# Performance work log

Measured on AMD Instinct MI355X. Metric: run time of the kernel, lower is better.

Reference implementation:

```python
import jax, jax.numpy as jnp
import numpy as np

NUM_KERNELS = 6
ALPHA = 0.5
DIL = 9
FEAT = 4
DELTA_V = 0.5
DELTA_D = 1.5
EMB_W = 0.25
MAX_LABELS = 16


def setup_inputs() -> dict:
    key = jax.random.key(0)
    k1, k2, k3, k4, k5 = jax.random.split(key, 5)
    B, H, W = 8, 640, 640
    pred = jax.random.normal(k1, (B, NUM_KERNELS + FEAT, H, W), dtype=jnp.float32)
    gt_text = (jax.random.uniform(k2, (B, 1, H, W)) < 0.3).astype(jnp.float32)
    gt_kernels = (jax.random.uniform(k3, (B, NUM_KERNELS - 1, H, W)) < 0.2).astype(jnp.float32)
    training_mask = (jax.random.uniform(k4, (B, 1, H, W)) > 0.05).astype(jnp.float32)
    gt_instance = jax.random.randint(k5, (B, H, W), 0, MAX_LABELS, dtype=jnp.int32)
    return {"pred": pred, "gt_text": gt_text, "gt_kernels": gt_kernels,
            "training_mask": training_mask, "gt_instance": gt_instance}


def _dice(inp, tgt, msk, eps=1e-6):
    # inp/tgt/msk: [N, HW]; returns mean over N of (1 - 2*I/U)
    inp = inp * msk
    tgt = tgt * msk
    inter = (inp * tgt).sum(1)
    union = (inp ** 2).sum(1) + (tgt ** 2).sum(1) + eps
    return (1.0 - 2.0 * inter / union).mean()


def _ohem(pred, gt, tm, ratio=3):
    # Vectorized OHEM: keep all positives + top-(3*n_pos) hardest negatives per sample.
    B = gt.shape[0]
    p = pred.reshape(B, -1)
    g = gt.reshape(B, -1)
    m = tm.reshape(B, -1)
    pos = (g > 0.5) & (m > 0.5)
    neg = (g <= 0.5) & (m > 0.5)
    n_pos = pos.sum(1)
    n_neg = jnp.minimum(ratio * n_pos, neg.sum(1))
    score = jnp.where(neg, p, -jnp.inf)
    # rank[i,j] = position of element j in descending order of score[i]
    rank = jnp.argsort(jnp.argsort(-score, axis=1), axis=1)
    mask = pos | (neg & (rank < n_neg[:, None]))
    return mask.astype(pred.dtype).reshape(gt.shape)


def _emb_sample(emb, gt, tm):
    # emb: [D,H,W], gt: [H,W] int, tm: [H,W]
    D = emb.shape[0]
    e = emb.reshape(D, -1).T                       # [HW, D]
    g = gt.reshape(-1)
    valid = tm.reshape(-1) > 0
    ids = jnp.where(valid, g, MAX_LABELS)          # invalid pixels -> dump segment
    ones = valid.astype(e.dtype)
    counts = jax.ops.segment_sum(ones, ids, num_segments=MAX_LABELS + 1)[:MAX_LABELS]
    sums = jax.ops.segment_sum(e * ones[:, None], ids, num_segments=MAX_LABELS + 1)[:MAX_LABELS]
    present = counts > 0
    n = present.sum()
    nf = n.astype(e.dtype)
    means = sums / jnp.maximum(counts, 1.0)[:, None]   # [L, D]
    # variance term: per-pixel distance to own cluster mean
    own = means[g]                                     # [HW, D]
    d = jnp.sqrt(((e - own) ** 2).sum(1) + 1e-12)
    cv = jnp.maximum(d - DELTA_V, 0.0) ** 2
    per = jax.ops.segment_sum(cv * ones, ids, num_segments=MAX_LABELS + 1)[:MAX_LABELS]
    per = per / jnp.maximum(counts, 1.0)
    lv = jnp.where(present, per, 0.0).sum() / jnp.maximum(nf, 1.0)
    # distance term: pairwise over present cluster means (unordered pairs i<j)
    diff = means[:, None, :] - means[None, :, :]
    pd = jnp.sqrt((diff ** 2).sum(-1) + 1e-12)
    iu = jnp.arange(MAX_LABELS)
    pm = present[:, None] & present[None, :] & (iu[:, None] < iu[None, :])
    ld = jnp.where(pm, jnp.maximum(2.0 * DELTA_D - pd, 0.0) ** 2, 0.0).sum()
    ld = ld / jnp.maximum(nf * (nf - 1.0), 1.0)
    # regularization: mean norm of present cluster means
    lr = jnp.where(present, jnp.sqrt((means ** 2).sum(1) + 1e-12), 0.0).sum() / jnp.maximum(nf, 1.0)
    act = (n > 1).astype(e.dtype)   # skip samples with <=1 instance (matches `continue`)
    return act * lv, act * ld, act * lr


def reference(pred, gt_text, gt_kernels, training_mask, gt_instance):
    B = pred.shape[0]
    gt_t = gt_text[:, 0]
    tm = training_mask[:, 0]
    # text branch: sigmoid -> 9x9 max-pool dilation -> OHEM dice
    prob = jax.nn.sigmoid(pred[:, 0])
    pad = DIL // 2
    dil = jax.lax.reduce_window(prob, -jnp.inf, jax.lax.max,
                                (1, DIL, DIL), (1, 1, 1),
                                [(0, 0), (pad, pad), (pad, pad)])
    ohem = jax.lax.stop_gradient(_ohem(dil, gt_t, tm, ratio=3))
    loss_text = _dice(dil.reshape(B, -1), gt_t.reshape(B, -1), ohem.reshape(B, -1))
    # kernel branch: mean over (B, K) equals sum_k dice_k / K
    K = NUM_KERNELS - 1
    pk = jax.nn.sigmoid(pred[:, 1:NUM_KERNELS]).reshape(B * K, -1)
    gk = gt_kernels.reshape(B * K, -1)
    mk = jnp.broadcast_to(tm[:, None], (B, K) + tm.shape[1:]).reshape(B * K, -1)
    loss_kernels = _dice(pk, gk, mk)
    # embedding clustering loss
    pred_emb = pred[:, NUM_KERNELS:]
    lv, ld, lr = jax.vmap(_emb_sample)(pred_emb, gt_instance, tm)
    loss_emb = EMB_W * (lv.sum() + ld.sum() + 0.001 * (lr.sum() / B))
    loss = loss_kernels + ALPHA * loss_text + loss_emb
    return loss, loss_text, loss_kernels, loss_emb
```

## Files before the change

### kernel.cpp

```cpp
#include <hip/hip_runtime.h>
#include <math.h>

#define BB 8
#define HH 640
#define WW 640
#define HWN (HH*WW)
#define CC 10
#define KCH 5
#define DD 4
#define LL 16
#define NBINS 256
#define ETILE 1024

#define WS_OHEM      0
#define WS_HCNT      64
#define WS_HS2       (WS_HCNT + BB*NBINS)
#define WS_KERN      (WS_HS2 + BB*NBINS)
#define WS_ECNT      (WS_KERN + 120)
#define WS_ESUM      (WS_ECNT + BB*LL)
#define WS_ECV       (WS_ESUM + BB*LL*DD)
#define WS_ZERO_END  (WS_ECV + BB)
#define WS_MEANS     WS_ZERO_END
#define WS_INVC      (WS_MEANS + BB*LL*DD)
#define WS_MISC      (WS_INVC + BB*LL)

typedef short bf16x8 __attribute__((ext_vector_type(8)));
typedef float f32x4  __attribute__((ext_vector_type(4)));

__device__ __forceinline__ float sigm(float x) { return 1.f / (1.f + expf(-x)); }

__device__ __forceinline__ float wave_red(float v) {
    #pragma unroll
    for (int o = 32; o > 0; o >>= 1) v += __shfl_down(v, o);
    return v;
}

__device__ __forceinline__ unsigned short f2bf(float x) {
    return (unsigned short)((__float_as_uint(x) + 0x8000u) >> 16);
}

__device__ __forceinline__ float4 ld4g(const float* __restrict__ p, int row, int cb) {
    float4 v;
    if (row < 0 || row >= HH) { v.x = v.y = v.z = v.w = -INFINITY; return v; }
    const float* rp = p + (size_t)row * WW;
    if (cb >= 0 && cb <= WW - 4) return *(const float4*)(rp + cb);
    v.x = ((unsigned)(cb + 0) < (unsigned)WW) ? rp[cb + 0] : -INFINITY;
    v.y = ((unsigned)(cb + 1) < (unsigned)WW) ? rp[cb + 1] : -INFINITY;
    v.z = ((unsigned)(cb + 2) < (unsigned)WW) ? rp[cb + 2] : -INFINITY;
    v.w = ((unsigned)(cb + 3) < (unsigned)WW) ? rp[cb + 3] : -INFINITY;
    return v;
}

__global__ __launch_bounds__(256) void k_dil_stats(
    const float* __restrict__ pred, const float* __restrict__ gt_t,
    const float* __restrict__ tm, float* __restrict__ ws)
{
    __shared__ float hmax[72][65];
    __shared__ float hcnt[2][NBINS];
    __shared__ float hs2[2][NBINS];
    __shared__ float red[8];
    const int b  = blockIdx.z;
    const int x0 = blockIdx.x * 64;
    const int y0 = blockIdx.y * 64;
    const int tid = threadIdx.x;
    const float* p0 = pred + (size_t)b * CC * HWN;

    for (int i = tid; i < 2 * NBINS; i += 256) {
        ((float*)hcnt)[i] = 0.f; ((float*)hs2)[i] = 0.f;
    }
    if (tid < 8) red[tid] = 0.f;

    for (int i = tid; i < 72 * 16; i += 256) {
        int r = i >> 4, g = i & 15;
        int gr = y0 + r - 4;
        int cb = x0 + 4 * g - 4;
        float4 A  = ld4g(p0, gr, cb);
        float4 Bv = ld4g(p0, gr, cb + 4);
        float4 Cv = ld4g(p0, gr, cb + 8);
        float s3 = A.w;
        float s2 = fmaxf(A.z, s3);
        float s1 = fmaxf(A.y, s2);
        float s0 = fmaxf(A.x, s1);
        float mid = fmaxf(fmaxf(Bv.x, Bv.y), fmaxf(Bv.z, Bv.w));
        float q0 = Cv.x;
        float q1 = fmaxf(q0, Cv.y);
        float q2 = fmaxf(q1, Cv.z);
        float q3 = fmaxf(q2, Cv.w);
        int c = 4 * g;
        hmax[r][c + 0] = fmaxf(fmaxf(s0, mid), q0);
        hmax[r][c + 1] = fmaxf(fmaxf(s1, mid), q1);
        hmax[r][c + 2] = fmaxf(fmaxf(s2, mid), q2);
        hmax[r][c + 3] = fmaxf(fmaxf(s3, mid), q3);
    }
    __syncthreads();

    const int c  = tid & 63;
    const int rb = tid >> 6;
    const int hc = tid >> 7;
    float c_pos = 0.f, s_pos = 0.f, s_pos2 = 0.f, c_neg = 0.f, s_neg2 = 0.f;
    #pragma unroll
    for (int k = 0; k < 16; k++) {
        int r = rb * 16 + k;
        float m = hmax[r][c];
        #pragma unroll
        for (int j = 1; j < 9; j++) m = fmaxf(m, hmax[r + j][c]);
        float dil = sigm(m);
        size_t gidx = (size_t)b * HWN + (size_t)(y0 + r) * WW + (x0 + c);
        float g = gt_t[gidx], mv = tm[gidx];
        if (mv > 0.5f) {
            if (g > 0.5f) { c_pos += 1.f; s_pos += dil; s_pos2 += dil * dil; }
            else {
                c_neg += 1.f; s_neg2 += dil * dil;
                int bin = (int)((m + 8.f) * 16.f);
                bin = min(max(bin, 0), NBINS - 1);
                atomicAdd(&hcnt[hc][bin], 1.f);
                atomicAdd(&hs2[hc][bin], dil * dil);
            }
        }
    }
    c_pos = wave_red(c_pos); s_pos = wave_red(s_pos); s_pos2 = wave_red(s_pos2);
    c_neg = wave_red(c_neg); s_neg2 = wave_red(s_neg2);
    if ((tid & 63) == 0) {
        atomicAdd(&red[0], c_pos);  atomicAdd(&red[1], s_pos);
        atomicAdd(&red[2], s_pos2); atomicAdd(&red[3], c_neg);
        atomicAdd(&red[4], s_neg2);
    }
    __syncthreads();
    float* oh = ws + WS_OHEM + b * 8;
    if (tid < 5) atomicAdd(&oh[tid], red[tid]);
    float* gh_c = ws + WS_HCNT + b * NBINS;
    float* gh_s = ws + WS_HS2  + b * NBINS;
    for (int i = tid; i < NBINS; i += 256) {
        float sc = hcnt[0][i] + hcnt[1][i];
        if (sc != 0.f) {
            atomicAdd(&gh_c[i], sc);
            atomicAdd(&gh_s[i], hs2[0][i] + hs2[1][i]);
        }
    }
}

__global__ __launch_bounds__(256) void k_kern_dice(
    const float* __restrict__ pred, const float* __restrict__ gtk,
    const float* __restrict__ tm, float* __restrict__ ws)
{
    const int row = blockIdx.y;
    const int b = row / KCH, k = row - b * KCH;
    const float4* p = (const float4*)(pred + ((size_t)b * CC + 1 + k) * HWN);
    const float4* g = (const float4*)(gtk + (size_t)row * HWN);
    const float4* m = (const float4*)(tm + (size_t)b * HWN);
    const int nv = HWN / 4;
    float i1 = 0.f, i2 = 0.f, i3 = 0.f;
    for (int j = blockIdx.x * 256 + threadIdx.x; j < nv; j += gridDim.x * 256) {
        float4 pv = p[j], gv = g[j], mv = m[j];
        float s0 = sigm(pv.x), s1 = sigm(pv.y), s2 = sigm(pv.z), s3 = sigm(pv.w);
        i1 += s0*gv.x*mv.x + s1*gv.y*mv.y + s2*gv.z*mv.z + s3*gv.w*mv.w;
        i2 += s0*s0*mv.x + s1*s1*mv.y + s2*s2*mv.z + s3*s3*mv.w;
        i3 += gv.x*mv.x + gv.y*mv.y + gv.z*mv.z + gv.w*mv.w;
    }
    i1 = wave_red(i1); i2 = wave_red(i2); i3 = wave_red(i3);
    __shared__ float sred[12];
    int wv = threadIdx.x >> 6;
    if ((threadIdx.x & 63) == 0) { sred[wv*3] = i1; sred[wv*3+1] = i2; sred[wv*3+2] = i3; }
    __syncthreads();
    if (threadIdx.x == 0) {
        float a = 0.f, bb = 0.f, c = 0.f;
        for (int w = 0; w < 4; w++) { a += sred[w*3]; bb += sred[w*3+1]; c += sred[w*3+2]; }
        float* kk = ws + WS_KERN + row * 3;
        atomicAdd(&kk[0], a); atomicAdd(&kk[1], bb); atomicAdd(&kk[2], c);
    }
}

__global__ __launch_bounds__(256) void k_emb1(
    const float* __restrict__ pred, const int* __restrict__ inst,
    const float* __restrict__ tm, float* __restrict__ ws)
{
    const int b = blockIdx.y;
    __shared__ unsigned short chs[4][ETILE + 16];
    __shared__ unsigned int   labv[ETILE];
    __shared__ float          merge[4 * 80];
    const int tid  = threadIdx.x;
    const int wave = tid >> 6, lane = tid & 63;
    const int q = lane >> 4, n = lane & 15;
    const float* e0  = pred + ((size_t)b * CC + 6) * HWN;
    const float* tmb = tm + (size_t)b * HWN;
    const int*   ib  = inst + (size_t)b * HWN;

    const bool isch = (n >= 1 && n <= 4);
    const int  cn   = isch ? (n - 1) : 0;

    f32x4 acc = {0.f, 0.f, 0.f, 0.f};

    for (int t0 = blockIdx.x * ETILE; t0 < HWN; t0 += gridDim.x * ETILE) {
        {
            int p = t0 + tid * 4;
            float4 T = *(const float4*)(tmb + p);
            int4   L = *(const int4*)(ib + p);
            #pragma unroll
            for (int c = 0; c < 4; c++) {
                float4 V = *(const float4*)(e0 + (size_t)c * HWN + p);
                unsigned short* dst = &chs[c][tid * 4];
                dst[0] = f2bf(V.x); dst[1] = f2bf(V.y);
                dst[2] = f2bf(V.z); dst[3] = f2bf(V.w);
            }
            uint4 lv;
            lv.x = (T.x > 0.f) ? (unsigned)L.x : 255u;
            lv.y = (T.y > 0.f) ? (unsigned)L.y : 255u;
            lv.z = (T.z > 0.f) ? (unsigned)L.z : 255u;
            lv.w = (T.w > 0.f) ? (unsigned)L.w : 255u;
            *(uint4*)&labv[tid * 4] = lv;
        }
        __syncthreads();

        for (int c2 = wave; c2 < ETILE / 32; c2 += 4) {
            const int base = c2 * 32 + q * 8;
            uint4 La = *(const uint4*)&labv[base];
            uint4 Lb = *(const uint4*)&labv[base + 4];
            union { unsigned short u[8]; bf16x8 v; } A_;
            const unsigned un = (unsigned)n;
            A_.u[0] = (La.x == un) ? 0x3F80 : 0;
            A_.u[1] = (La.y == un) ? 0x3F80 : 0;
            A_.u[2] = (La.z == un) ? 0x3F80 : 0;
            A_.u[3] = (La.w == un) ? 0x3F80 : 0;
            A_.u[4] = (Lb.x == un) ? 0x3F80 : 0;
            A_.u[5] = (Lb.y == un) ? 0x3F80 : 0;
            A_.u[6] = (Lb.z == un) ? 0x3F80 : 0;
            A_.u[7] = (Lb.w == un) ? 0x3F80 : 0;
            bf16x8 Bf;
            if (isch) {
                Bf = *(const bf16x8*)&chs[cn][base];
            } else if (n == 0) {
                #pragma unroll
                for (int j = 0; j < 8; j++) Bf[j] = (short)0x3F80;
            } else {
                #pragma unroll
                for (int j = 0; j < 8; j++) Bf[j] = 0;
            }
            acc = __builtin_amdgcn_mfma_f32_16x16x32_bf16(A_.v, Bf, acc, 0, 0, 0);
        }
        __syncthreads();
    }

    if (n <= 4) {
        #pragma unroll
        for (int r = 0; r < 4; r++)
            merge[wave * 80 + (q * 4 + r) * 5 + n] = acc[r];
    }
    __syncthreads();
    if (tid < 80) {
        float s = merge[tid] + merge[80 + tid] + merge[160 + tid] + merge[240 + tid];
        int l = tid / 5, c = tid - l * 5;
        if (c == 0) atomicAdd(&ws[WS_ECNT + b * LL + l], s);
        else        atomicAdd(&ws[WS_ESUM + b * LL * DD + l * DD + (c - 1)], s);
    }
}

__global__ __launch_bounds__(128) void k_emb_means(float* __restrict__ ws)
{
    const int b = blockIdx.x;
    __shared__ float mn[LL][DD];
    __shared__ float pres[LL];
    __shared__ float redp[128];
    __shared__ float redr[LL];
    const int tid = threadIdx.x;
    if (tid < LL) {
        float c = ws[WS_ECNT + b * LL + tid];
        float inv = 1.f / fmaxf(c, 1.f);
        ws[WS_INVC + b * LL + tid] = inv;
        #pragma unroll
        for (int d = 0; d < DD; d++) {
            float mv = ws[WS_ESUM + b * LL * DD + tid * DD + d] * inv;
            mn[tid][d] = mv;
            ws[WS_MEANS + b * LL * DD + tid * DD + d] = mv;
        }
        pres[tid] = (c > 0.f) ? 1.f : 0.f;
    }
    __syncthreads();
    float ldv = 0.f;
    if (tid < 120) {
        int idx = tid, ii = 0;
        while (idx >= (LL - 1 - ii)) { idx -= (LL - 1 - ii); ii++; }
        int jj = ii + 1 + idx;
        float s = 1e-12f;
        #pragma unroll
        for (int d = 0; d < DD; d++) { float df = mn[ii][d] - mn[jj][d]; s += df * df; }
        float pd = sqrtf(s);
        float t = fmaxf(3.0f - pd, 0.f);
        ldv = (pres[ii] > 0.f && pres[jj] > 0.f) ? t * t : 0.f;
    }
    redp[tid] = ldv;
    float lrv = 0.f;
    if (tid < LL && pres[tid] > 0.f) {
        float s = 1e-12f;
        #pragma unroll
        for (int d = 0; d < DD; d++) s += mn[tid][d] * mn[tid][d];
        lrv = sqrtf(s);
    }
    if (tid < LL) redr[tid] = lrv;
    __syncthreads();
    if (tid == 0) {
        float nf = 0.f;
        for (int i = 0; i < LL; i++) nf += pres[i];
        float ld = 0.f;
        for (int i = 0; i < 120; i++) ld += redp[i];
        float lr = 0.f;
        for (int i = 0; i < LL; i++) lr += redr[i];
        float act = (nf > 1.f) ? 1.f : 0.f;
        ld = act * ld / fmaxf(nf * (nf - 1.f), 1.f);
        lr = act * lr / fmaxf(nf, 1.f);
        ws[WS_MISC + b * 4 + 0] = nf;
        ws[WS_MISC + b * 4 + 1] = ld;
        ws[WS_MISC + b * 4 + 2] = lr;
        ws[WS_MISC + b * 4 + 3] = act;
    }
}

__global__ __launch_bounds__(256) void k_emb2(
    const float* __restrict__ pred, const int* __restrict__ inst,
    const float* __restrict__ tm, float* __restrict__ ws)
{
    const int b = blockIdx.y;
    const int tid = threadIdx.x;
    __shared__ float mn[LL * DD];
    __shared__ float invc[LL];
    if (tid < LL * DD) mn[tid] = ws[WS_MEANS + b * LL * DD + tid];
    if (tid < LL) invc[tid] = ws[WS_INVC + b * LL + tid];
    __syncthreads();

    const float* e0 = pred + ((size_t)b * CC + 6) * HWN;
    const float4* v0p = (const float4*)e0;
    const float4* v1p = (const float4*)(e0 + HWN);
    const float4* v2p = (const float4*)(e0 + 2 * HWN);
    const float4* v3p = (const float4*)(e0 + 3 * HWN);
    const float4* tmv = (const float4*)(tm + (size_t)b * HWN);
    const int4*   iv  = (const int4*)(inst + (size_t)b * HWN);

    float acc = 0.f;
    const int nv = HWN / 4;
    for (int j = blockIdx.x * 256 + tid; j < nv; j += gridDim.x * 256) {
        float4 a0 = v0p[j], a1 = v1p[j], a2 = v2p[j], a3 = v3p[j];
        float4 t = tmv[j];
        int4 li = iv[j];
        float ex[4] = {a0.x, a0.y, a0.z, a0.w};
        float ey[4] = {a1.x, a1.y, a1.z, a1.w};
        float ez[4] = {a2.x, a2.y, a2.z, a2.w};
        float ew[4] = {a3.x, a3.y, a3.z, a3.w};
        int   lb[4] = {li.x, li.y, li.z, li.w};
        float tv[4] = {t.x, t.y, t.z, t.w};
        #pragma unroll
        for (int qq = 0; qq < 4; qq++) {
            int l = lb[qq];
            float d0 = ex[qq] - mn[l * DD + 0];
            float d1 = ey[qq] - mn[l * DD + 1];
            float d2 = ez[qq] - mn[l * DD + 2];
            float d3 = ew[qq] - mn[l * DD + 3];
            float dd = sqrtf(d0*d0 + d1*d1 + d2*d2 + d3*d3 + 1e-12f);
            float tt = fmaxf(dd - 0.5f, 0.f);
            float w = (tv[qq] > 0.f) ? invc[l] : 0.f;
            acc += w * tt * tt;
        }
    }

    acc = wave_red(acc);
    __shared__ float sred[4];
    const int wv = tid >> 6;
    if ((tid & 63) == 0) sred[wv] = acc;
    __syncthreads();
    if (tid == 0)
        atomicAdd(&ws[WS_ECV + b], sred[0] + sred[1] + sred[2] + sred[3]);
}

__global__ __launch_bounds__(64) void k_final(const float* __restrict__ ws, float* __restrict__ out)
{
    __shared__ float s_text[BB];
    __shared__ float s_kern[40];
    __shared__ float s_lv[BB], s_ld[BB], s_lr[BB];
    const int tid = threadIdx.x;
    if (tid < BB) {
        const float* o = ws + WS_OHEM + tid * 8;
        float npos = o[0], spos = o[1], spos2 = o[2], nnegt = o[3], sneg2t = o[4];
        float nneg = fminf(3.f * npos, nnegt);
        float ssel;
        if (nneg >= nnegt) ssel = sneg2t;
        else {
            const float* hcn = ws + WS_HCNT + tid * NBINS;
            const float* hs = ws + WS_HS2  + tid * NBINS;
            float acc = 0.f; ssel = 0.f;
            for (int i = NBINS - 1; i >= 0; i--) {
                float c = hcn[i];
                if (c <= 0.f) continue;
                if (acc + c <= nneg) { ssel += hs[i]; acc += c; }
                else { float r = nneg - acc; ssel += r * (hs[i] / c); break; }
            }
        }
        float uni = spos2 + ssel + npos + 1e-6f;
        s_text[tid] = 1.f - 2.f * spos / uni;

        float nf  = ws[WS_MISC + tid * 4 + 0];
        float act = ws[WS_MISC + tid * 4 + 3];
        s_lv[tid] = act * ws[WS_ECV + tid] / fmaxf(nf, 1.f);
        s_ld[tid] = ws[WS_MISC + tid * 4 + 1];
        s_lr[tid] = ws[WS_MISC + tid * 4 + 2];
    }
    if (tid < 40) {
        const float* kk = ws + WS_KERN + tid * 3;
        s_kern[tid] = 1.f - 2.f * kk[0] / (kk[1] + kk[2] + 1e-6f);
    }
    __syncthreads();
    if (tid == 0) {
        float lt = 0.f; for (int i = 0; i < BB; i++) lt += s_text[i]; lt /= (float)BB;
        float lk = 0.f; for (int i = 0; i < 40; i++) lk += s_kern[i]; lk /= 40.f;
        float lvs = 0.f, lds_ = 0.f, lrs = 0.f;
        for (int i = 0; i < BB; i++) { lvs += s_lv[i]; lds_ += s_ld[i]; lrs += s_lr[i]; }
        float lemb = 0.25f * (lvs + lds_ + 0.001f * (lrs / (float)BB));
        out[0] = lk + 0.5f * lt + lemb;
        out[1] = lt;
        out[2] = lk;
        out[3] = lemb;
    }
}

extern "C" void kernel_launch(void* const* d_in, const int* in_sizes, int n_in,
                              void* d_out, int out_size, void* d_ws, size_t ws_size,
                              hipStream_t stream)
{
    (void)in_sizes; (void)n_in; (void)out_size; (void)ws_size;
    const float* pred = (const float*)d_in[0];
    const float* gt_t = (const float*)d_in[1];
    const float* gtk  = (const float*)d_in[2];
    const float* tm   = (const float*)d_in[3];
    const int*   inst = (const int*)d_in[4];
    float* out = (float*)d_out;
    float* ws  = (float*)d_ws;

    hipMemsetAsync(d_ws, 0, WS_ZERO_END * sizeof(float), stream);

    dim3 g1(WW / 64, HH / 64, BB), b1(256, 1, 1);
    k_dil_stats<<<g1, b1, 0, stream>>>(pred, gt_t, tm, ws);
    k_kern_dice<<<dim3(48, 40), 256, 0, stream>>>(pred, gtk, tm, ws);
    k_emb1<<<dim3(64, BB), 256, 0, stream>>>(pred, inst, tm, ws);
    k_emb_means<<<BB, 128, 0, stream>>>(ws);
    k_emb2<<<dim3(128, BB), 256, 0, stream>>>(pred, inst, tm, ws);
    k_final<<<1, 64, 0, stream>>>(ws, out);
}
```

Measured before the change: 338.1 us.

## Share mask loads across kernel channels and fold emb_means into emb2/final

The kernel-dice pass now handles all five kernel channels per batch in one block, so the training mask is loaded once per pixel instead of five times, and the grid becomes 96x8. The separate k_emb_means launch is removed: k_emb2 computes means and inverse counts itself, and k_final computes the pairwise distance and regularization terms in shared memory. Sigmoid switches to the fast __expf intrinsic. This cuts mask traffic and one launch, at the cost of more registers per thread and slightly different floating-point summation order.

```diff
diff --git a/kernel.cpp b/kernel.cpp
--- a/kernel.cpp
+++ b/kernel.cpp
@@ -20,14 +20,11 @@
 #define WS_ESUM      (WS_ECNT + BB*LL)
 #define WS_ECV       (WS_ESUM + BB*LL*DD)
 #define WS_ZERO_END  (WS_ECV + BB)
-#define WS_MEANS     WS_ZERO_END
-#define WS_INVC      (WS_MEANS + BB*LL*DD)
-#define WS_MISC      (WS_INVC + BB*LL)
 
 typedef short bf16x8 __attribute__((ext_vector_type(8)));
 typedef float f32x4  __attribute__((ext_vector_type(4)));
 
-__device__ __forceinline__ float sigm(float x) { return 1.f / (1.f + expf(-x)); }
+__device__ __forceinline__ float sigm(float x) { return 1.f / (1.f + __expf(-x)); }
 
 __device__ __forceinline__ float wave_red(float v) {
     #pragma unroll
@@ -143,30 +140,45 @@
     const float* __restrict__ pred, const float* __restrict__ gtk,
     const float* __restrict__ tm, float* __restrict__ ws)
 {
-    const int row = blockIdx.y;
-    const int b = row / KCH, k = row - b * KCH;
-    const float4* p = (const float4*)(pred + ((size_t)b * CC + 1 + k) * HWN);
-    const float4* g = (const float4*)(gtk + (size_t)row * HWN);
+    const int b = blockIdx.y;
+    const float* pb = pred + ((size_t)b * CC + 1) * HWN;
+    const float* gb = gtk + (size_t)b * KCH * HWN;
     const float4* m = (const float4*)(tm + (size_t)b * HWN);
     const int nv = HWN / 4;
-    float i1 = 0.f, i2 = 0.f, i3 = 0.f;
+    float i1[KCH], i2[KCH], i3[KCH];
+    #pragma unroll
+    for (int c = 0; c < KCH; c++) { i1[c] = 0.f; i2[c] = 0.f; i3[c] = 0.f; }
+
     for (int j = blockIdx.x * 256 + threadIdx.x; j < nv; j += gridDim.x * 256) {
-        float4 pv = p[j], gv = g[j], mv = m[j];
-        float s0 = sigm(pv.x), s1 = sigm(pv.y), s2 = sigm(pv.z), s3 = sigm(pv.w);
-        i1 += s0*gv.x*mv.x + s1*gv.y*mv.y + s2*gv.z*mv.z + s3*gv.w*mv.w;
-        i2 += s0*s0*mv.x + s1*s1*mv.y + s2*s2*mv.z + s3*s3*mv.w;
-        i3 += gv.x*mv.x + gv.y*mv.y + gv.z*mv.z + gv.w*mv.w;
-    }
-    i1 = wave_red(i1); i2 = wave_red(i2); i3 = wave_red(i3);
-    __shared__ float sred[12];
-    int wv = threadIdx.x >> 6;
-    if ((threadIdx.x & 63) == 0) { sred[wv*3] = i1; sred[wv*3+1] = i2; sred[wv*3+2] = i3; }
-    __syncthreads();
-    if (threadIdx.x == 0) {
-        float a = 0.f, bb = 0.f, c = 0.f;
-        for (int w = 0; w < 4; w++) { a += sred[w*3]; bb += sred[w*3+1]; c += sred[w*3+2]; }
-        float* kk = ws + WS_KERN + row * 3;
-        atomicAdd(&kk[0], a); atomicAdd(&kk[1], bb); atomicAdd(&kk[2], c);
+        float4 mv = m[j];
+        #pragma unroll
+        for (int c = 0; c < KCH; c++) {
+            float4 pv = ((const float4*)(pb + (size_t)c * HWN))[j];
+            float4 gv = ((const float4*)(gb + (size_t)c * HWN))[j];
+            float s0 = sigm(pv.x), s1 = sigm(pv.y), s2 = sigm(pv.z), s3 = sigm(pv.w);
+            i1[c] += s0*gv.x*mv.x + s1*gv.y*mv.y + s2*gv.z*mv.z + s3*gv.w*mv.w;
+            i2[c] += s0*s0*mv.x + s1*s1*mv.y + s2*s2*mv.z + s3*s3*mv.w;
+            i3[c] += gv.x*mv.x + gv.y*mv.y + gv.z*mv.z + gv.w*mv.w;
+        }
+    }
+
+    __shared__ float sred[4][15];
+    const int wv = threadIdx.x >> 6;
+    #pragma unroll
+    for (int c = 0; c < KCH; c++) {
+        float r1 = wave_red(i1[c]);
+        float r2 = wave_red(i2[c]);
+        float r3 = wave_red(i3[c]);
+        if ((threadIdx.x & 63) == 0) {
+            sred[wv][c*3+0] = r1; sred[wv][c*3+1] = r2; sred[wv][c*3+2] = r3;
+        }
+    }
+    __syncthreads();
+    if (threadIdx.x < 15) {
+        float s = sred[0][threadIdx.x] + sred[1][threadIdx.x]
+                + sred[2][threadIdx.x] + sred[3][threadIdx.x];
+        int c = threadIdx.x / 3, jj = threadIdx.x - c * 3;
+        atomicAdd(&ws[WS_KERN + (b * KCH + c) * 3 + jj], s);
     }
 }
 
@@ -254,66 +266,6 @@
     }
 }
 
-__global__ __launch_bounds__(128) void k_emb_means(float* __restrict__ ws)
-{
-    const int b = blockIdx.x;
-    __shared__ float mn[LL][DD];
-    __shared__ float pres[LL];
-    __shared__ float redp[128];
-    __shared__ float redr[LL];
-    const int tid = threadIdx.x;
-    if (tid < LL) {
-        float c = ws[WS_ECNT + b * LL + tid];
-        float inv = 1.f / fmaxf(c, 1.f);
-        ws[WS_INVC + b * LL + tid] = inv;
-        #pragma unroll
-        for (int d = 0; d < DD; d++) {
-            float mv = ws[WS_ESUM + b * LL * DD + tid * DD + d] * inv;
-            mn[tid][d] = mv;
-            ws[WS_MEANS + b * LL * DD + tid * DD + d] = mv;
-        }
-        pres[tid] = (c > 0.f) ? 1.f : 0.f;
-    }
-    __syncthreads();
-    float ldv = 0.f;
-    if (tid < 120) {
-        int idx = tid, ii = 0;
-        while (idx >= (LL - 1 - ii)) { idx -= (LL - 1 - ii); ii++; }
-        int jj = ii + 1 + idx;
-        float s = 1e-12f;
-        #pragma unroll
-        for (int d = 0; d < DD; d++) { float df = mn[ii][d] - mn[jj][d]; s += df * df; }
-        float pd = sqrtf(s);
-        float t = fmaxf(3.0f - pd, 0.f);
-        ldv = (pres[ii] > 0.f && pres[jj] > 0.f) ? t * t : 0.f;
-    }
-    redp[tid] = ldv;
-    float lrv = 0.f;
-    if (tid < LL && pres[tid] > 0.f) {
-        float s = 1e-12f;
-        #pragma unroll
-        for (int d = 0; d < DD; d++) s += mn[tid][d] * mn[tid][d];
-        lrv = sqrtf(s);
-    }
-    if (tid < LL) redr[tid] = lrv;
-    __syncthreads();
-    if (tid == 0) {
-        float nf = 0.f;
-        for (int i = 0; i < LL; i++) nf += pres[i];
-        float ld = 0.f;
-        for (int i = 0; i < 120; i++) ld += redp[i];
-        float lr = 0.f;
-        for (int i = 0; i < LL; i++) lr += redr[i];
-        float act = (nf > 1.f) ? 1.f : 0.f;
-        ld = act * ld / fmaxf(nf * (nf - 1.f), 1.f);
-        lr = act * lr / fmaxf(nf, 1.f);
-        ws[WS_MISC + b * 4 + 0] = nf;
-        ws[WS_MISC + b * 4 + 1] = ld;
-        ws[WS_MISC + b * 4 + 2] = lr;
-        ws[WS_MISC + b * 4 + 3] = act;
-    }
-}
-
 __global__ __launch_bounds__(256) void k_emb2(
     const float* __restrict__ pred, const int* __restrict__ inst,
     const float* __restrict__ tm, float* __restrict__ ws)
@@ -322,8 +274,15 @@
     const int tid = threadIdx.x;
     __shared__ float mn[LL * DD];
     __shared__ float invc[LL];
-    if (tid < LL * DD) mn[tid] = ws[WS_MEANS + b * LL * DD + tid];
-    if (tid < LL) invc[tid] = ws[WS_INVC + b * LL + tid];
+    if (tid < LL) {
+        float c = ws[WS_ECNT + b * LL + tid];
+        invc[tid] = 1.f / fmaxf(c, 1.f);
+    }
+    __syncthreads();
+    if (tid < LL * DD) {
+        int l = tid >> 2;
+        mn[tid] = ws[WS_ESUM + b * LL * DD + tid] * invc[l];
+    }
     __syncthreads();
 
     const float* e0 = pred + ((size_t)b * CC + 6) * HWN;
@@ -369,12 +328,53 @@
         atomicAdd(&ws[WS_ECV + b], sred[0] + sred[1] + sred[2] + sred[3]);
 }
 
-__global__ __launch_bounds__(64) void k_final(const float* __restrict__ ws, float* __restrict__ out)
-{
+__global__ __launch_bounds__(256) void k_final(const float* __restrict__ ws, float* __restrict__ out)
+{
+    __shared__ float mn[BB][LL][DD];
+    __shared__ float pres[BB][LL];
+    __shared__ float nfa[BB], lda[BB], lra[BB];
     __shared__ float s_text[BB];
     __shared__ float s_kern[40];
     __shared__ float s_lv[BB], s_ld[BB], s_lr[BB];
     const int tid = threadIdx.x;
+    if (tid < BB) { nfa[tid] = 0.f; lda[tid] = 0.f; lra[tid] = 0.f; }
+    __syncthreads();
+    if (tid < BB * LL) {
+        int b = tid >> 4, l = tid & 15;
+        float c = ws[WS_ECNT + b * LL + l];
+        float inv = 1.f / fmaxf(c, 1.f);
+        #pragma unroll
+        for (int d = 0; d < DD; d++)
+            mn[b][l][d] = ws[WS_ESUM + b * LL * DD + l * DD + d] * inv;
+        float p = (c > 0.f) ? 1.f : 0.f;
+        pres[b][l] = p;
+        atomicAdd(&nfa[b], p);
+    }
+    __syncthreads();
+    for (int t = tid; t < BB * 120; t += 256) {
+        int b = t / 120, idx = t - b * 120, ii = 0;
+        while (idx >= (LL - 1 - ii)) { idx -= (LL - 1 - ii); ii++; }
+        int jj = ii + 1 + idx;
+        if (pres[b][ii] > 0.f && pres[b][jj] > 0.f) {
+            float s = 1e-12f;
+            #pragma unroll
+            for (int d = 0; d < DD; d++) {
+                float df = mn[b][ii][d] - mn[b][jj][d]; s += df * df;
+            }
+            float tt = fmaxf(3.0f - sqrtf(s), 0.f);
+            if (tt > 0.f) atomicAdd(&lda[b], tt * tt);
+        }
+    }
+    if (tid < BB * LL) {
+        int b = tid >> 4, l = tid & 15;
+        if (pres[b][l] > 0.f) {
+            float s = 1e-12f;
+            #pragma unroll
+            for (int d = 0; d < DD; d++) s += mn[b][l][d] * mn[b][l][d];
+            atomicAdd(&lra[b], sqrtf(s));
+        }
+    }
+    __syncthreads();
     if (tid < BB) {
         const float* o = ws + WS_OHEM + tid * 8;
         float npos = o[0], spos = o[1], spos2 = o[2], nnegt = o[3], sneg2t = o[4];
@@ -395,11 +395,11 @@
         float uni = spos2 + ssel + npos + 1e-6f;
         s_text[tid] = 1.f - 2.f * spos / uni;
 
-        float nf  = ws[WS_MISC + tid * 4 + 0];
-        float act = ws[WS_MISC + tid * 4 + 3];
+        float nf  = nfa[tid];
+        float act = (nf > 1.f) ? 1.f : 0.f;
         s_lv[tid] = act * ws[WS_ECV + tid] / fmaxf(nf, 1.f);
-        s_ld[tid] = ws[WS_MISC + tid * 4 + 1];
-        s_lr[tid] = ws[WS_MISC + tid * 4 + 2];
+        s_ld[tid] = act * lda[tid] / fmaxf(nf * (nf - 1.f), 1.f);
+        s_lr[tid] = act * lra[tid] / fmaxf(nf, 1.f);
     }
     if (tid < 40) {
         const float* kk = ws + WS_KERN + tid * 3;
@@ -436,9 +436,8 @@
 
     dim3 g1(WW / 64, HH / 64, BB), b1(256, 1, 1);
     k_dil_stats<<<g1, b1, 0, stream>>>(pred, gt_t, tm, ws);
-    k_kern_dice<<<dim3(48, 40), 256, 0, stream>>>(pred, gtk, tm, ws);
+    k_kern_dice<<<dim3(96, BB), 256, 0, stream>>>(pred, gtk, tm, ws);
     k_emb1<<<dim3(64, BB), 256, 0, stream>>>(pred, inst, tm, ws);
-    k_emb_means<<<BB, 128, 0, stream>>>(ws);
     k_emb2<<<dim3(128, BB), 256, 0, stream>>>(pred, inst, tm, ws);
-    k_final<<<1, 64, 0, stream>>>(ws, out);
-}
+    k_final<<<1, 256, 0, stream>>>(ws, out);
+}
```

New measurement: 333.5 us. No clear change (-1.4%).
